# Optimization experiments

Hardware: AMD Instinct MI355X
Metric: run time of the kernel (lower is better)

## Reference

```python
import jax, jax.numpy as jnp
import numpy as np

L, D, H, N, B2 = 9, 256, 4, 1024, 4   # layers, embed dim, heads, keypoints, 2*pairs
HD = D // H
THR = 0.1
MAXM = 50


def _linear(x, W, b):
    return x @ W.T + b


def _ln(x, g, b, eps=1e-5):
    m = jnp.mean(x, -1, keepdims=True)
    v = jnp.var(x, -1, keepdims=True)
    return (x - m) * jax.lax.rsqrt(v + eps) * g + b


def _ffn(x, w1, b1, g, bb, w2, b2):
    h = _linear(x, w1, b1)
    h = jax.nn.gelu(_ln(h, g, bb), approximate=False)
    return _linear(h, w2, b2)


def _mha(q, k, v):
    b, nq, _ = q.shape
    nk = k.shape[1]
    qh = q.reshape(b, nq, H, HD)
    kh = k.reshape(b, nk, H, HD)
    vh = v.reshape(b, nk, H, HD)
    s = jnp.einsum('bqhd,bkhd->bhqk', qh, kh) * (1.0 / np.float32(np.sqrt(HD)))
    a = jax.nn.softmax(s, -1)
    return jnp.einsum('bhqk,bkhd->bqhd', a, vh).reshape(b, nq, D)


def _rotate_half(qk):  # qk: [b, n, D, 2]
    b, n, _, _ = qk.shape
    r = qk.reshape(b, n, H, HD // 2, 2, 2)
    r = jnp.stack([-r[..., 1, :], r[..., 0, :]], axis=4)
    return r.reshape(b, n, D, 2)


def _posenc(kpts, Wr):
    proj = kpts @ Wr.T                    # [b, n, HD//2]
    def expand(t):
        t = jnp.repeat(t, 2, axis=-1)     # interleave -> [b, n, HD]
        return jnp.tile(t, (1, 1, H))     # -> [b, n, D]
    return jnp.stack([expand(jnp.cos(proj)), expand(jnp.sin(proj))])  # [2, b, n, D]


def _forward(kpts, desc, posenc_Wr,
             sWqkv_w, sWqkv_b, sOut_w, sOut_b, sF1_w, sF1_b, sLN_g, sLN_b, sF2_w, sF2_b,
             cQK_w, cQK_b, cV_w, cV_b, cOut_w, cOut_b, cF1_w, cF1_b, cLN_g, cLN_b, cF2_w, cF2_b,
             fp_w, fp_b, match_w, match_b):
    enc = _posenc(kpts, posenc_Wr)
    x = desc
    idx = np.arange(B2)
    swap = idx // 2 * 2 + (1 - idx % 2)   # swap images within each pair
    for i in range(L):
        # ---- self attention with cached rotary encoding ----
        b, n, _ = x.shape
        qkv = _linear(x, sWqkv_w[i], sWqkv_b[i]).reshape(b, n, D, 3)
        qk, v = qkv[..., :2], qkv[..., 2]
        qk = enc[0][..., None] * qk + enc[1][..., None] * _rotate_half(qk)
        ctx = _mha(qk[..., 0], qk[..., 1], v)
        msg = _linear(ctx, sOut_w[i], sOut_b[i])
        x = x + _ffn(jnp.concatenate([x, msg], -1),
                     sF1_w[i], sF1_b[i], sLN_g[i], sLN_b[i], sF2_w[i], sF2_b[i])
        # ---- cross attention between images of each pair ----
        qk = _linear(x, cQK_w[i], cQK_b[i])
        v = _linear(x, cV_w[i], cV_b[i])
        m = _mha(qk, qk[swap], v[swap])
        m = _linear(m, cOut_w[i], cOut_b[i])
        x = x + _ffn(jnp.concatenate([x, m], -1),
                     cF1_w[i], cF1_b[i], cLN_g[i], cLN_b[i], cF2_w[i], cF2_b[i])
    # ---- match assignment: sigmoid log double softmax ----
    md = _linear(x, fp_w, fp_b) / (D ** 0.25)
    sim = jnp.einsum('bnd,bmd->bnm', md[0::2], md[1::2])
    z = _linear(x, match_w, match_b)      # [B2, N, 1]
    cert = jax.nn.log_sigmoid(z[0::2]) + jnp.swapaxes(jax.nn.log_sigmoid(z[1::2]), 1, 2)
    return jax.nn.log_softmax(sim, 2) + jax.nn.log_softmax(sim, 1) + cert


def _filter_matches(scores):
    B = scores.shape[0]
    m0 = jnp.argmax(scores, 2)
    m1 = jnp.argmax(scores, 1)
    mscores = jnp.exp(jnp.max(scores, 2))
    mutual = jnp.arange(N)[None, :] == jnp.take_along_axis(m1, m0, 1)
    masked = mscores * ((mscores > THR) & mutual).astype(mscores.dtype)
    topk_scores, topk_idx = jax.lax.top_k(masked, MAXM)
    topk_m1 = jnp.take_along_axis(m0, topk_idx, 1)
    b_idx = jnp.broadcast_to(jnp.arange(B)[:, None], (B, MAXM))
    matches = jnp.stack([b_idx, topk_idx, topk_m1], 2)
    return matches[0], topk_scores[0]


def setup_inputs() -> dict:
    key = jax.random.key(0)
    ks = iter(jax.random.split(key, 48))
    def w(shape, scale=0.02):
        return jax.random.normal(next(ks), shape, jnp.float32) * scale
    inp = {
        'kpts': jax.random.normal(next(ks), (B2, N, 2), jnp.float32),
        'desc': jax.random.normal(next(ks), (B2, N, D), jnp.float32),
        'posenc_Wr': w((HD // 2, 2), 1.0),  # std = gamma**-2 = 1
        'sWqkv_w': w((L, 3 * D, D)), 'sWqkv_b': w((L, 3 * D)),
        'sOut_w': w((L, D, D)), 'sOut_b': w((L, D)),
        'sF1_w': w((L, 2 * D, 2 * D)), 'sF1_b': w((L, 2 * D)),
        'sLN_g': jnp.ones((L, 2 * D), jnp.float32), 'sLN_b': jnp.zeros((L, 2 * D), jnp.float32),
        'sF2_w': w((L, D, 2 * D)), 'sF2_b': w((L, D)),
        'cQK_w': w((L, D, D)), 'cQK_b': w((L, D)),
        'cV_w': w((L, D, D)), 'cV_b': w((L, D)),
        'cOut_w': w((L, D, D)), 'cOut_b': w((L, D)),
        'cF1_w': w((L, 2 * D, 2 * D)), 'cF1_b': w((L, 2 * D)),
        'cLN_g': jnp.ones((L, 2 * D), jnp.float32), 'cLN_b': jnp.zeros((L, 2 * D), jnp.float32),
        'cF2_w': w((L, D, 2 * D)), 'cF2_b': w((L, D)),
        'fp_w': w((D, D)), 'fp_b': w((D,)),
        'match_w': w((1, D)), 'match_b': w((1,)),
    }
    return inp


def reference(kpts, desc, posenc_Wr,
              sWqkv_w, sWqkv_b, sOut_w, sOut_b, sF1_w, sF1_b, sLN_g, sLN_b, sF2_w, sF2_b,
              cQK_w, cQK_b, cV_w, cV_b, cOut_w, cOut_b, cF1_w, cF1_b, cLN_g, cLN_b, cF2_w, cF2_b,
              fp_w, fp_b, match_w, match_b):
    scores = _forward(kpts, desc, posenc_Wr,
                      sWqkv_w, sWqkv_b, sOut_w, sOut_b, sF1_w, sF1_b, sLN_g, sLN_b, sF2_w, sF2_b,
                      cQK_w, cQK_b, cV_w, cV_b, cOut_w, cOut_b, cF1_w, cF1_b, cLN_g, cLN_b, cF2_w, cF2_b,
                      fp_w, fp_b, match_w, match_b)
    matches, mscores = _filter_matches(scores)
    return scores, matches, mscores
```

## Files before the change

### kernel.cpp

```cpp
#include <hip/hip_runtime.h>
#include <hip/hip_bf16.h>
#include <math.h>

typedef __hip_bfloat16 bf16;
typedef unsigned short ushort;
typedef unsigned int u32;
typedef __attribute__((ext_vector_type(8))) short s8b;
typedef __attribute__((ext_vector_type(4))) short s4b;
typedef __attribute__((ext_vector_type(4))) float f4v;

#define Nc 1024
#define Dc 256
#define MA 4096

__device__ __forceinline__ float tofl(float v){ return v; }
__device__ __forceinline__ float tofl(bf16 v){ return __bfloat162float(v); }

__device__ __forceinline__ ushort rneu(float f){
  unsigned u = __float_as_uint(f);
  unsigned r = (u + 0x7fffu + ((u>>16)&1u)) >> 16;
  return (ushort)r;
}
__device__ __forceinline__ float ubf(ushort h){ return __uint_as_float(((unsigned)h)<<16); }

__device__ __forceinline__ float fexp2(float x){
#if __has_builtin(__builtin_amdgcn_exp2f)
  return __builtin_amdgcn_exp2f(x);
#else
  return exp2f(x);
#endif
}

__global__ void k_detect(const void* p, int* flag){
  if(threadIdx.x==0 && blockIdx.x==0){
    *flag = (((const ushort*)p)[0] == 0x3F80) ? 0 : 1;
  }
}

template<typename TIN>
__device__ void gemm_body(const float* A, const TIN* B, const TIN* bias, float* C,
                          int M, int Nout, int K, int lda, int ldb, int ldc,
                          float alpha, int accum, int dolog){
  __shared__ float As[32][33];
  __shared__ float Bs[32][33];
  int tx = threadIdx.x, ty = threadIdx.y;
  int tid = ty*16 + tx;
  int n0 = blockIdx.x*32, m0 = blockIdx.y*32;
  int lr = tid >> 3;
  int lc = (tid & 7) * 4;
  float acc00=0.f, acc01=0.f, acc10=0.f, acc11=0.f;
  for(int kk=0; kk<K; kk+=32){
    int m = m0 + lr, n = n0 + lr;
#pragma unroll
    for(int j=0;j<4;j++){
      int k = kk + lc + j;
      As[lr][lc+j] = (m < M && k < K) ? A[(size_t)m*lda + k] : 0.f;
      Bs[lr][lc+j] = (n < Nout && k < K) ? tofl(B[(size_t)n*ldb + k]) : 0.f;
    }
    __syncthreads();
#pragma unroll
    for(int k=0;k<32;k++){
      float a0 = As[ty][k],   a1 = As[ty+16][k];
      float b0 = Bs[tx][k],   b1 = Bs[tx+16][k];
      acc00 += a0*b0; acc01 += a0*b1; acc10 += a1*b0; acc11 += a1*b1;
    }
    __syncthreads();
  }
#define STORE(mm,nn,acc) do{ int m_=(mm), n_=(nn); if(m_<M && n_<Nout){ \
    float r = (acc) + (bias ? tofl(bias[n_]) : 0.f); r *= alpha; \
    if(dolog) r = fminf(r,0.f) - log1pf(expf(-fabsf(r))); \
    if(accum) C[(size_t)m_*ldc + n_] += r; else C[(size_t)m_*ldc + n_] = r; } }while(0)
  STORE(m0+ty,    n0+tx,    acc00);
  STORE(m0+ty,    n0+tx+16, acc01);
  STORE(m0+ty+16, n0+tx,    acc10);
  STORE(m0+ty+16, n0+tx+16, acc11);
#undef STORE
}

__global__ __launch_bounds__(256)
void k_gemm_w(const int* flag, const float* A, const void* Bb, long boff,
              const void* biasb, long biasoff, float* C,
              int M, int Nout, int K, int lda, int ldb, int ldc,
              float alpha, int accum, int dolog){
  if(*flag){
    const float* B = ((const float*)Bb) + boff;
    const float* bi = biasb ? ((const float*)biasb) + biasoff : nullptr;
    gemm_body<float>(A, B, bi, C, M, Nout, K, lda, ldb, ldc, alpha, accum, dolog);
  }else{
    const bf16* B = ((const bf16*)Bb) + boff;
    const bf16* bi = biasb ? ((const bf16*)biasb) + biasoff : nullptr;
    gemm_body<bf16>(A, B, bi, C, M, Nout, K, lda, ldb, ldc, alpha, accum, dolog);
  }
}

template<typename TIN>
__device__ void cast2_body(const void* in_, float* x, ushort* xh, ushort* xl, int n){
  const TIN* in = (const TIN*)in_;
  int i = blockIdx.x*256 + threadIdx.x;
  if(i >= n) return;
  float f = tofl(in[i]);
  x[i] = f;
  ushort h = rneu(f);
  xh[i] = h; xl[i] = rneu(f - ubf(h));
}
__global__ void k_cast2(const int* flag, const void* in, float* x, ushort* xh, ushort* xl, int n){
  if(*flag) cast2_body<float>(in, x, xh, xl, n); else cast2_body<bf16>(in, x, xh, xl, n);
}

template<typename TIN>
__device__ void splitw_body(const void* src_, long off, ushort* dh, ushort* dl, int n){
  const TIN* src = ((const TIN*)src_) + off;
  int i = blockIdx.x*256 + threadIdx.x;
  if(i >= n) return;
  float f = tofl(src[i]);
  ushort h = rneu(f);
  dh[i] = h; dl[i] = rneu(f - ubf(h));
}
__global__ void k_splitw(const int* flag, const void* src, long off, ushort* dh, ushort* dl, int n){
  if(*flag) splitw_body<float>(src, off, dh, dl, n); else splitw_body<bf16>(src, off, dh, dl, n);
}
template<typename TIN>
__device__ void biasf_body(const void* src_, long off, float* dst, int n){
  const TIN* src = ((const TIN*)src_) + off;
  int i = blockIdx.x*256 + threadIdx.x;
  if(i < n) dst[i] = tofl(src[i]);
}
__global__ void k_biasf(const int* flag, const void* src, long off, float* dst, int n){
  if(*flag) biasf_body<float>(src, off, dst, n); else biasf_body<bf16>(src, off, dst, n);
}

template<typename TIN>
__device__ void rotcs_body(const void* kpts_, const void* Wr_, float* cs){
  int i = blockIdx.x*256 + threadIdx.x;
  if(i >= MA*32) return;
  int m = i >> 5, p = i & 31;
  const TIN* kpts = (const TIN*)kpts_;
  const TIN* Wr   = (const TIN*)Wr_;
  float kx = tofl(kpts[m*2]), ky = tofl(kpts[m*2+1]);
  float proj = kx*tofl(Wr[p*2]) + ky*tofl(Wr[p*2+1]);
  cs[(size_t)m*64 + p*2    ] = cosf(proj);
  cs[(size_t)m*64 + p*2 + 1] = sinf(proj);
}
__global__ void k_rotcs(const int* flag, const void* kpts, const void* Wr, float* cs){
  if(*flag) rotcs_body<float>(kpts, Wr, cs); else rotcs_body<bf16>(kpts, Wr, cs);
}

template<typename TIN>
__device__ void wsl_body(int L, const void* p0,const void* p1,const void* p2,const void* p3,
                         const void* p4,const void* p5,const void* p6,const void* p7,const void* p8,
                         const void* b0,const void* b1,const void* b2,const void* b3,const void* b4,
                         const void* b5,const void* b6,const void* b7,const void* b8,
                         ushort* WH, ushort* WL, float* WB){
  int idx = blockIdx.x*256 + threadIdx.x;
  if(idx < 311296){
    int i = idx*4;
    const TIN* s;
    if(i < 196608){
      int nr = i >> 8, col = i & 255;
      int sr = (nr < 256) ? nr*3 : (nr < 512) ? (nr-256)*3+1 : (nr-512)*3+2;
      s = (const TIN*)p0 + (size_t)L*196608 + sr*256 + col;
    }
    else if(i < 262144)  s = (const TIN*)p1 + (size_t)L*65536  + (i-196608);
    else if(i < 524288)  s = (const TIN*)p2 + (size_t)L*262144 + (i-262144);
    else if(i < 655360)  s = (const TIN*)p3 + (size_t)L*131072 + (i-524288);
    else if(i < 720896)  s = (const TIN*)p4 + (size_t)L*65536  + (i-655360);
    else if(i < 786432)  s = (const TIN*)p5 + (size_t)L*65536  + (i-720896);
    else if(i < 851968)  s = (const TIN*)p6 + (size_t)L*65536  + (i-786432);
    else if(i < 1114112) s = (const TIN*)p7 + (size_t)L*262144 + (i-851968);
    else                 s = (const TIN*)p8 + (size_t)L*131072 + (i-1114112);
    float f[4];
    if constexpr(sizeof(TIN) == 4){
      f4v v = *(const f4v*)s;
      f[0]=v[0]; f[1]=v[1]; f[2]=v[2]; f[3]=v[3];
    } else {
      s4b v = *(const s4b*)s;
#pragma unroll
      for(int j=0;j<4;j++) f[j] = __uint_as_float(((u32)(ushort)v[j])<<16);
    }
    s4b hv, lv;
#pragma unroll
    for(int j=0;j<4;j++){
      ushort h = rneu(f[j]);
      hv[j] = (short)h;
      lv[j] = (short)rneu(f[j] - ubf(h));
    }
    *(s4b*)&WH[i] = hv;
    *(s4b*)&WL[i] = lv;
  } else if(idx < 311296 + 3328){
    int j = idx - 311296;
    const TIN* s;
    if(j < 768){
      int sj = (j < 256) ? j*3 : (j < 512) ? (j-256)*3+1 : (j-512)*3+2;
      s = (const TIN*)b0 + (size_t)L*768 + sj;
    }
    else if(j < 1024)  s = (const TIN*)b1 + (size_t)L*256 + (j-768);
    else if(j < 1536)  s = (const TIN*)b2 + (size_t)L*512 + (j-1024);
    else if(j < 1792)  s = (const TIN*)b3 + (size_t)L*256 + (j-1536);
    else if(j < 2048)  s = (const TIN*)b4 + (size_t)L*256 + (j-1792);
    else if(j < 2304)  s = (const TIN*)b5 + (size_t)L*256 + (j-2048);
    else if(j < 2560)  s = (const TIN*)b6 + (size_t)L*256 + (j-2304);
    else if(j < 3072)  s = (const TIN*)b7 + (size_t)L*512 + (j-2560);
    else               s = (const TIN*)b8 + (size_t)L*256 + (j-3072);
    WB[j] = tofl(*s);
  }
}
__global__ void k_wsplit(const int* flag, int L0, long strW, long strB,
    const void* p0,const void* p1,const void* p2,const void* p3,const void* p4,
    const void* p5,const void* p6,const void* p7,const void* p8,
    const void* b0,const void* b1,const void* b2,const void* b3,const void* b4,
    const void* b5,const void* b6,const void* b7,const void* b8,
    ushort* WH, ushort* WL, float* WB){
  int L = L0 + blockIdx.y;
  ushort* WHl = WH + (size_t)blockIdx.y*strW;
  ushort* WLl = WL + (size_t)blockIdx.y*strW;
  float*  WBl = WB + (size_t)blockIdx.y*strB;
  if(*flag) wsl_body<float>(L,p0,p1,p2,p3,p4,p5,p6,p7,p8,b0,b1,b2,b3,b4,b5,b6,b7,b8,WHl,WLl,WBl);
  else      wsl_body<bf16>(L,p0,p1,p2,p3,p4,p5,p6,p7,p8,b0,b1,b2,b3,b4,b5,b6,b7,b8,WHl,WLl,WBl);
}

__global__ __launch_bounds__(256)
void k_wcomb(ushort* WH, ushort* WL, float* WB, long strW, long strB){
  __shared__ __align__(16) float w1b[16][256];
  int strip = blockIdx.x;
  int c = blockIdx.y;
  int L = c >> 1, br = c & 1;
  size_t wbase = (size_t)L*strW + (br ? 851968 : 262144);
  size_t obase = (size_t)L*strW + (br ? 786432 : 196608);
  float* WBl  = WB + (size_t)L*strB;
  float* b1   = WBl + (br ? 2560 : 1024);
  float* bout = WBl + (br ? 2304 : 768);
  int t = threadIdx.x;
  int o0 = strip*16;
  for(int idx = t; idx < 16*256; idx += 256){
    int o = idx >> 8, j = idx & 255;
    size_t s = wbase + (size_t)(o0+o)*512 + 256 + j;
    w1b[o][j] = ubf(WH[s]) + ubf(WL[s]);
  }
  __syncthreads();
  float acc[16];
#pragma unroll
  for(int o=0;o<16;o++) acc[o] = 0.f;
  for(int j=0;j<256;j+=8){
    size_t s0 = obase + (size_t)j*256 + t;
    float wv[8];
#pragma unroll
    for(int r=0;r<8;r++){
      wv[r] = ubf(WH[s0 + r*256]) + ubf(WL[s0 + r*256]);
    }
#pragma unroll
    for(int o=0;o<16;o++){
      f4v wa = *(const f4v*)&w1b[o][j];
      f4v wb = *(const f4v*)&w1b[o][j+4];
      acc[o] += wa[0]*wv[0] + wa[1]*wv[1] + wa[2]*wv[2] + wa[3]*wv[3]
              + wb[0]*wv[4] + wb[1]*wv[5] + wb[2]*wv[6] + wb[3]*wv[7];
    }
  }
#pragma unroll
  for(int o=0;o<16;o++){
    size_t s = wbase + (size_t)(o0+o)*512 + 256 + t;
    ushort hh = rneu(acc[o]);
    WH[s] = hh; WL[s] = rneu(acc[o] - ubf(hh));
  }
  if(t < 16){
    float s = 0.f;
    for(int j=0;j<256;j++) s += w1b[t][j]*bout[j];
    b1[o0 + t] += s;
  }
}

template<int MT>
__global__ __launch_bounds__(256)
void k_gemm_mxT(const ushort* __restrict__ Ah, const ushort* __restrict__ Al,
                const ushort* __restrict__ A2h, const ushort* __restrict__ A2l, int lda,
                const ushort* __restrict__ Bh, const ushort* __restrict__ Bl, int ldb,
                const float* __restrict__ bias, float alpha,
                float* C, int ldc, int accum,
                ushort* Ch, ushort* Cl, int lds,
                ushort* keh, ushort* kel, const float* __restrict__ cs,
                ushort* vth, ushort* vtl,
                int K, int mode){
  constexpr int MFR = MT/16;
  constexpr int NACC = MFR*2;
  constexpr int MFH = MFR/2;
  __shared__ __align__(16) ushort LB[(2*MT+128)*72];
  int t = threadIdx.x;
  int n0 = blockIdx.x*64, m0 = blockIdx.y*MT;
  int w = t>>6, lane = t&63, quad = lane>>4, l15 = lane&15;
  int kg = w>>1, nh = w&1;
  int brow = t>>2, bc16 = (t&3)*16;
  int arow = (MT==64) ? (t>>2) : (t>>3);
  int acol = (MT==64) ? ((t&3)*16) : ((t&7)*8);
  f4v acc[NACC];
  f4v zz = {0.f,0.f,0.f,0.f};
#pragma unroll
  for(int j=0;j<NACC;j++) acc[j] = zz;
  int rounds = K >> 6;

  s8b r0,r1,r2,r3,r4,r5,r6,r7;
  auto gload = [&](int r){
    int k0 = r*64;
    const ushort* ah = Ah; const ushort* al = Al; int kloc = k0;
    if(A2h && k0 >= 256){ ah = A2h; al = A2l; kloc = k0 - 256; }
    const ushort* aph = &ah[(size_t)(m0+arow)*lda + kloc + acol];
    const ushort* apl = &al[(size_t)(m0+arow)*lda + kloc + acol];
    const ushort* bph = &Bh[(size_t)(n0+brow)*ldb + k0 + bc16];
    const ushort* bpl = &Bl[(size_t)(n0+brow)*ldb + k0 + bc16];
    r0 = *(const s8b*)aph;
    r2 = *(const s8b*)apl;
    if(MT==64){ r1 = *(const s8b*)(aph+8); r3 = *(const s8b*)(apl+8); }
    r4 = *(const s8b*)bph;   r5 = *(const s8b*)(bph+8);
    r6 = *(const s8b*)bpl;   r7 = *(const s8b*)(bpl+8);
  };
  auto writeS = [&](){
    *(s8b*)&LB[(arow)*72 + acol]        = r0;
    *(s8b*)&LB[(MT+arow)*72 + acol]     = r2;
    if(MT==64){
      *(s8b*)&LB[(arow)*72 + acol+8]    = r1;
      *(s8b*)&LB[(MT+arow)*72 + acol+8] = r3;
    }
    *(s8b*)&LB[(2*MT+brow)*72 + bc16]      = r4;
    *(s8b*)&LB[(2*MT+brow)*72 + bc16+8]    = r5;
    *(s8b*)&LB[(2*MT+64+brow)*72 + bc16]   = r6;
    *(s8b*)&LB[(2*MT+64+brow)*72 + bc16+8] = r7;
  };

  gload(0);
  for(int r=0; r<rounds; r++){
    __syncthreads();
    writeS();
    __syncthreads();
    s8b afh[MFR], afl[MFR], bfh[2], bfl[2];
#pragma unroll
    for(int mf=0;mf<MFR;mf++){
      afh[mf] = *(s8b*)&LB[(mf*16+l15)*72 + kg*32+quad*8];
      afl[mf] = *(s8b*)&LB[(MT+mf*16+l15)*72 + kg*32+quad*8];
    }
#pragma unroll
    for(int nf=0;nf<2;nf++){
      bfh[nf] = *(s8b*)&LB[(2*MT+nh*32+nf*16+l15)*72 + kg*32+quad*8];
      bfl[nf] = *(s8b*)&LB[(2*MT+64+nh*32+nf*16+l15)*72 + kg*32+quad*8];
    }
    if(r+1 < rounds) gload(r+1);
#pragma unroll
    for(int mf=0;mf<MFR;mf++){
#pragma unroll
      for(int nf=0;nf<2;nf++){
        int a = mf*2+nf;
        acc[a] = __builtin_amdgcn_mfma_f32_16x16x32_bf16(afh[mf], bfh[nf], acc[a], 0,0,0);
        acc[a] = __builtin_amdgcn_mfma_f32_16x16x32_bf16(afh[mf], bfl[nf], acc[a], 0,0,0);
        acc[a] = __builtin_amdgcn_mfma_f32_16x16x32_bf16(afl[mf], bfh[nf], acc[a], 0,0,0);
      }
    }
  }
  __syncthreads();
  f4v* scr = (f4v*)LB;
#pragma unroll
  for(int f=0;f<NACC;f++) scr[(w*NACC+f)*64 + lane] = acc[f];
  __syncthreads();
  int pw = w^2;
#pragma unroll
  for(int f=0;f<NACC;f++){
    f4v o = scr[(pw*NACC+f)*64 + lane];
    acc[f] += o;
  }

  bool vblk = (mode == 1 && n0 >= 512) || (mode == 3 && n0 >= 256);
  if(vblk){
    __syncthreads();
    u32* tp = (u32*)LB;
#pragma unroll
    for(int mi=0;mi<MFH;mi++){
      int mf = kg*MFH + mi;
#pragma unroll
      for(int nf=0;nf<2;nf++){
        f4v a = acc[mf*2+nf];
#pragma unroll
        for(int rr=0;rr<4;rr++){
          int ml = mf*16 + quad*4 + rr;
          int nl = nh*32 + nf*16 + l15;
          float val = a[rr];
          if(bias) val += bias[n0 + nl];
          val *= alpha;
          ushort hh = rneu(val);
          ushort ll = rneu(val - ubf(hh));
          tp[nl*(MT+1) + ml] = (u32)hh | ((u32)ll << 16);
        }
      }
    }
    __syncthreads();
    int b = m0 >> 10;
    int mloc = m0 & 1023;
    int d0 = n0 - ((mode == 1) ? 512 : 256);
    constexpr int NPASS = (MT==64) ? 2 : 1;
#pragma unroll
    for(int pass=0; pass<NPASS; pass++){
      int row, col;
      if(MT==64){ row = (t>>3) + pass*32; col = (t&7)*8; }
      else      { row = t>>2;             col = (t&3)*8; }
      int d = d0 + row;
      u32 c0=tp[row*(MT+1)+col+0], c1=tp[row*(MT+1)+col+1], c2=tp[row*(MT+1)+col+2], c3=tp[row*(MT+1)+col+3];
      u32 c4=tp[row*(MT+1)+col+4], c5=tp[row*(MT+1)+col+5], c6=tp[row*(MT+1)+col+6], c7=tp[row*(MT+1)+col+7];
      s8b hi, lo;
      hi[0]=(short)(c0&0xffff); lo[0]=(short)(c0>>16);
      hi[1]=(short)(c1&0xffff); lo[1]=(short)(c1>>16);
      hi[2]=(short)(c2&0xffff); lo[2]=(short)(c2>>16);
      hi[3]=(short)(c3&0xffff); lo[3]=(short)(c3>>16);
      hi[4]=(short)(c4&0xffff); lo[4]=(short)(c4>>16);
      hi[5]=(short)(c5&0xffff); lo[5]=(short)(c5>>16);
      hi[6]=(short)(c6&0xffff); lo[6]=(short)(c6>>16);
      hi[7]=(short)(c7&0xffff); lo[7]=(short)(c7>>16);
      size_t go = ((size_t)((b*4 + (d>>6))*64 + (d&63)))*1024 + mloc + col;
      *(s8b*)&vth[go] = hi;
      *(s8b*)&vtl[go] = lo;
    }
    return;
  }

#pragma unroll
  for(int mi=0;mi<MFH;mi++){
    int mf = kg*MFH + mi;
#pragma unroll
    for(int nf=0;nf<2;nf++){
      f4v a = acc[mf*2+nf];
#pragma unroll
      for(int rr=0;rr<4;rr++){
        int m = m0 + mf*16 + quad*4 + rr;
        int n = n0 + nh*32 + nf*16 + l15;
        float val = a[rr];
        if(bias) val += bias[n];
        val *= alpha;
        if(mode == 1){
          int d = (n < 256) ? n : (n - 256);
          const float* csp = cs + (size_t)m*64 + (d & 62);
          float cc = csp[0], ssn = csp[1];
          float pv = __shfl_xor(val, 1);
          float rv = (d & 1) ? (cc*val + ssn*pv) : (cc*val - ssn*pv);
          ushort hh = rneu(rv);
          ushort* dh = (n < 256) ? Ch : keh;
          ushort* dl = (n < 256) ? Cl : kel;
          size_t gi = (size_t)m*256 + d;
          dh[gi] = hh; dl[gi] = rneu(rv - ubf(hh));
        } else if(mode == 3){
          ushort hh = rneu(val);
          Ch[(size_t)m*256 + n] = hh;
          Cl[(size_t)m*256 + n] = rneu(val - ubf(hh));
        } else {
          if(C){
            size_t ci = (size_t)m*ldc + n;
            if(accum) val += C[ci];
            C[ci] = val;
          }
          if(Ch){
            ushort hh = rneu(val);
            Ch[(size_t)m*lds + n] = hh;
            Cl[(size_t)m*lds + n] = rneu(val - ubf(hh));
          }
        }
      }
    }
  }
}

#define FSC 0.18033688011112042f
__global__ __launch_bounds__(256)
void k_flashmx(const ushort* __restrict__ qh_, const ushort* __restrict__ ql_,
               const ushort* __restrict__ kh_, const ushort* __restrict__ kl_,
               const ushort* __restrict__ vth_, const ushort* __restrict__ vtl_,
               ushort* __restrict__ cth, ushort* __restrict__ ctl, int bxor,
               float* __restrict__ PO, float* __restrict__ PML, int nch){
  int qt = blockIdx.x, z = blockIdx.y, ch = blockIdx.z;
  int b = z>>2, h = z&3;
  int bk = b ^ bxor;
  __shared__ __align__(16) ushort Kh[64][72], Kl[64][72], Vh[64][72], Vl[64][72];
  int t = threadIdx.x, w = t>>6, lane = t&63, quad = lane>>4, l15 = lane&15;
  ushort* Psw = &Kh[w*16][0];
  s8b qfh[2], qfl[2];
  {
    size_t row = (size_t)b*1024 + qt*64 + w*16 + l15;
    const ushort* qrh = qh_ + row*256 + h*64;
    const ushort* qrl = ql_ + row*256 + h*64;
    qfh[0] = *(const s8b*)(qrh + quad*8);
    qfh[1] = *(const s8b*)(qrh + 32 + quad*8);
    qfl[0] = *(const s8b*)(qrl + quad*8);
    qfl[1] = *(const s8b*)(qrl + 32 + quad*8);
  }
  float m_i[4] = {-1e30f,-1e30f,-1e30f,-1e30f};
  float l_i[4] = {0.f,0.f,0.f,0.f};
  f4v O[4];
  f4v zz = {0.f,0.f,0.f,0.f};
#pragma unroll
  for(int dt=0;dt<4;dt++) O[dt] = zz;

  s8b rK0,rK1,rK2,rK3, rV0,rV1,rV2,rV3;
  auto stage_load = [&](int kt){
#pragma unroll
    for(int i=0;i<4;i++){
      int c = t + i*256;
      int half = c>>9, row = (c>>3)&63, o8 = (c&7)*8;
      const s8b* src = (const s8b*)((half ? kl_ : kh_) +
                       ((size_t)(bk*1024 + kt*64 + row))*256 + h*64 + o8);
      if(i==0) rK0=*src; else if(i==1) rK1=*src; else if(i==2) rK2=*src; else rK3=*src;
    }
#pragma unroll
    for(int i=0;i<4;i++){
      int c = t + i*256;
      int half = c>>9, d = (c>>3)&63, o8 = (c&7)*8;
      const s8b* src = (const s8b*)((half ? vtl_ : vth_) +
                       ((size_t)((bk*4+h)*64 + d))*1024 + kt*64 + o8);
      if(i==0) rV0=*src; else if(i==1) rV1=*src; else if(i==2) rV2=*src; else rV3=*src;
    }
  };
  auto stage_write = [&](){
#pragma unroll
    for(int i=0;i<4;i++){
      int c = t + i*256;
      int half = c>>9, row = (c>>3)&63, o8 = (c&7)*8;
      s8b v = (i==0)?rK0:(i==1)?rK1:(i==2)?rK2:rK3;
      if(half) *(s8b*)&Kl[row][o8] = v;
      else     *(s8b*)&Kh[row][o8] = v;
    }
#pragma unroll
    for(int i=0;i<4;i++){
      int c = t + i*256;
      int half = c>>9, d = (c>>3)&63, o8 = (c&7)*8;
      s8b v = (i==0)?rV0:(i==1)?rV1:(i==2)?rV2:rV3;
      if(half) *(s8b*)&Vl[d][o8] = v;
      else     *(s8b*)&Vh[d][o8] = v;
    }
  };

  int ktn = 16/nch;
  int kt0 = ch*ktn;
  stage_load(kt0);
  for(int kt=kt0; kt<kt0+ktn; kt++){
    __syncthreads();
    stage_write();
    __syncthreads();
    if(kt+1 < kt0+ktn) stage_load(kt+1);
    f4v s[4];
#pragma unroll
    for(int nt=0;nt<4;nt++) s[nt] = zz;
#pragma unroll
    for(int nt=0;nt<4;nt++){
#pragma unroll
      for(int k2=0;k2<2;k2++){
        s8b fbh = *(s8b*)&Kh[nt*16+l15][k2*32 + quad*8];
        s8b fbl = *(s8b*)&Kl[nt*16+l15][k2*32 + quad*8];
        s[nt] = __builtin_amdgcn_mfma_f32_16x16x32_bf16(qfh[k2], fbh, s[nt], 0,0,0);
        s[nt] = __builtin_amdgcn_mfma_f32_16x16x32_bf16(qfh[k2], fbl, s[nt], 0,0,0);
        s[nt] = __builtin_amdgcn_mfma_f32_16x16x32_bf16(qfl[k2], fbh, s[nt], 0,0,0);
      }
    }
    __syncthreads();
#pragma unroll
    for(int rr=0;rr<4;rr++){
      float v0=s[0][rr]*FSC, v1=s[1][rr]*FSC, v2=s[2][rr]*FSC, v3=s[3][rr]*FSC;
      float mx = fmaxf(fmaxf(v0,v1), fmaxf(v2,v3));
      mx = fmaxf(mx, __shfl_xor(mx,1));
      mx = fmaxf(mx, __shfl_xor(mx,2));
      mx = fmaxf(mx, __shfl_xor(mx,4));
      mx = fmaxf(mx, __shfl_xor(mx,8));
      float mnew = fmaxf(m_i[rr], mx);
      float al = fexp2(m_i[rr] - mnew);
      float p0 = fexp2(v0-mnew), p1 = fexp2(v1-mnew), p2 = fexp2(v2-mnew), p3 = fexp2(v3-mnew);
      float ls = p0+p1+p2+p3;
      ls += __shfl_xor(ls,1);
      ls += __shfl_xor(ls,2);
      ls += __shfl_xor(ls,4);
      ls += __shfl_xor(ls,8);
      l_i[rr] = l_i[rr]*al + ls;
      m_i[rr] = mnew;
#pragma unroll
      for(int dt=0;dt<4;dt++) O[dt][rr] *= al;
      int prow = quad*4 + rr;
      Psw[prow*72 +  0 + l15] = rneu(p0);
      Psw[prow*72 + 16 + l15] = rneu(p1);
      Psw[prow*72 + 32 + l15] = rneu(p2);
      Psw[prow*72 + 48 + l15] = rneu(p3);
    }
    s8b pf0 = *(s8b*)&Psw[l15*72 + quad*8];
    s8b pf1 = *(s8b*)&Psw[l15*72 + 32 + quad*8];
#pragma unroll
    for(int dt=0;dt<4;dt++){
#pragma unroll
      for(int k2=0;k2<2;k2++){
        s8b fvh = *(s8b*)&Vh[dt*16+l15][k2*32 + quad*8];
        s8b fvl = *(s8b*)&Vl[dt*16+l15][k2*32 + quad*8];
        s8b pf = k2 ? pf1 : pf0;
        O[dt] = __builtin_amdgcn_mfma_f32_16x16x32_bf16(pf, fvh, O[dt], 0,0,0);
        O[dt] = __builtin_amdgcn_mfma_f32_16x16x32_bf16(pf, fvl, O[dt], 0,0,0);
      }
    }
  }
  if(nch == 1){
#pragma unroll
    for(int rr=0;rr<4;rr++){
      float inv = 1.f / l_i[rr];
      int row = qt*64 + w*16 + quad*4 + rr;
#pragma unroll
      for(int dt=0;dt<4;dt++){
        float val = O[dt][rr]*inv;
        size_t gi = ((size_t)b*1024 + row)*256 + h*64 + dt*16 + l15;
        ushort hh = rneu(val);
        cth[gi] = hh; ctl[gi] = rneu(val - ubf(hh));
      }
    }
  } else {
    size_t tb = (size_t)(z*16+qt)*nch + ch;
    float* po  = PO  + tb*4096;
    float* pml = PML + tb*128;
#pragma unroll
    for(int rr=0;rr<4;rr++){
      int row = w*16 + quad*4 + rr;
#pragma unroll
      for(int dt=0;dt<4;dt++){
        po[row*64 + dt*16 + l15] = O[dt][rr];
      }
      if(l15 == 0){
        pml[row]      = m_i[rr];
        pml[64 + row] = l_i[rr];
      }
    }
  }
}

__global__ __launch_bounds__(256)
void k_fmerge(const float* __restrict__ PO, const float* __restrict__ PML,
              ushort* __restrict__ cth, ushort* __restrict__ ctl){
  int qt = blockIdx.x, z = blockIdx.y;
  int b = z>>2, h = z&3;
  int t = threadIdx.x;
  int row = t>>2, dg = (t&3)*16;
  size_t tb0 = (size_t)(z*16+qt)*4;
  float m0 = PML[(tb0+0)*128 + row], m1 = PML[(tb0+1)*128 + row];
  float m2 = PML[(tb0+2)*128 + row], m3 = PML[(tb0+3)*128 + row];
  float M = fmaxf(fmaxf(m0,m1), fmaxf(m2,m3));
  float w0 = fexp2(m0-M), w1 = fexp2(m1-M), w2 = fexp2(m2-M), w3 = fexp2(m3-M);
  float L = PML[(tb0+0)*128 + 64 + row]*w0 + PML[(tb0+1)*128 + 64 + row]*w1
          + PML[(tb0+2)*128 + 64 + row]*w2 + PML[(tb0+3)*128 + 64 + row]*w3;
  float inv = 1.f/L;
  const f4v* p0 = (const f4v*)(PO + (tb0+0)*4096 + row*64 + dg);
  const f4v* p1 = (const f4v*)(PO + (tb0+1)*4096 + row*64 + dg);
  const f4v* p2 = (const f4v*)(PO + (tb0+2)*4096 + row*64 + dg);
  const f4v* p3 = (const f4v*)(PO + (tb0+3)*4096 + row*64 + dg);
  size_t gi = ((size_t)b*1024 + qt*64 + row)*256 + h*64 + dg;
#pragma unroll
  for(int j=0;j<4;j++){
    f4v o = p0[j]*w0 + p1[j]*w1 + p2[j]*w2 + p3[j]*w3;
#pragma unroll
    for(int e=0;e<4;e++){
      float val = o[e]*inv;
      ushort hh = rneu(val);
      cth[gi + j*4 + e] = hh;
      ctl[gi + j*4 + e] = rneu(val - ubf(hh));
    }
  }
}

template<typename TIN>
__device__ void ln2_body(const float* h, ushort* hh, ushort* hl, const TIN* g, const TIN* bb){
  __shared__ float ws8[8];
  int r = blockIdx.x; int t = threadIdx.x;
  int w = t>>6, lane = t&63;
  const float* row = h + (size_t)r*512;
  float a = row[t], b_ = row[t+256];
  float s = a + b_;
#pragma unroll
  for(int off=1; off<64; off<<=1) s += __shfl_xor(s, off);
  if(lane==0) ws8[w] = s;
  __syncthreads();
  float mean = (ws8[0]+ws8[1]+ws8[2]+ws8[3])*(1.f/512.f);
  float da = a-mean, db = b_-mean;
  float v = da*da + db*db;
#pragma unroll
  for(int off=1; off<64; off<<=1) v += __shfl_xor(v, off);
  if(lane==0) ws8[4+w] = v;
  __syncthreads();
  float rstd = rsqrtf((ws8[4]+ws8[5]+ws8[6]+ws8[7])*(1.f/512.f) + 1e-5f);
  float na = da*rstd*tofl(g[t])     + tofl(bb[t]);
  float nb = db*rstd*tofl(g[t+256]) + tofl(bb[t+256]);
  float ga = 0.5f*na*(1.f + erff(na*0.70710678f));
  float gb = 0.5f*nb*(1.f + erff(nb*0.70710678f));
  size_t base = (size_t)r*512;
  ushort u0 = rneu(ga); hh[base+t] = u0; hl[base+t] = rneu(ga - ubf(u0));
  ushort u1 = rneu(gb); hh[base+t+256] = u1; hl[base+t+256] = rneu(gb - ubf(u1));
}
__global__ void k_ln_gelu2(const int* flag, const float* h, ushort* hh, ushort* hl,
                           const void* gb, long goff, const void* bbb, long boff){
  if(*flag) ln2_body<float>(h, hh, hl, ((const float*)gb)+goff, ((const float*)bbb)+boff);
  else      ln2_body<bf16>(h, hh, hl, ((const bf16*)gb)+goff, ((const bf16*)bbb)+boff);
}

__global__ void k_lse_cols2(const float* __restrict__ simbase, float* __restrict__ clseb){
  __shared__ float Rm[16][16], Rs[16][16];
  int blk = blockIdx.x;
  int p = blk >> 6, bx = blk & 63;
  const float* sim = simbase + (size_t)p*1048576;
  float* clse = clseb + p*1024;
  int t = threadIdx.x;
  int c = t & 15, s = t >> 4;
  int col = bx*16 + c;
  const float* base = sim + col;
  float mx = -1e30f, sum = 0.f;
  for(int n=s*64; n<s*64+64; n++){
    float v = base[(size_t)n*1024];
    if(v > mx){ sum = sum*expf(mx - v) + 1.f; mx = v; }
    else sum += expf(v - mx);
  }
  Rm[s][c] = mx; Rs[s][c] = sum; __syncthreads();
  for(int off=8; off>0; off>>=1){
    if(s < off){
      float m2 = Rm[s+off][c], s2 = Rs[s+off][c];
      float m1 = Rm[s][c], s1 = Rs[s][c];
      float m = fmaxf(m1, m2);
      Rm[s][c] = m;
      Rs[s][c] = s1*expf(m1-m) + s2*expf(m2-m);
    }
    __syncthreads();
  }
  if(s == 0) clse[col] = Rm[0][c] + logf(Rs[0][c]);
}

__global__ __launch_bounds__(256)
void k_final2r(float* __restrict__ out,
               const float* __restrict__ clse, const float* __restrict__ lsg,
               int* __restrict__ m0, float* __restrict__ msc){
  __shared__ float ws4[4];
  __shared__ float bsum[4];
  int blk = blockIdx.x;
  int p = blk >> 10, n = blk & 1023;
  int t = threadIdx.x;
  int w = t>>6, lane = t&63;
  size_t base = (size_t)blk*1024;
  float v0 = out[base+t], v1 = out[base+t+256], v2 = out[base+t+512], v3 = out[base+t+768];
  float mx = fmaxf(fmaxf(v0,v1),fmaxf(v2,v3));
#pragma unroll
  for(int off=1; off<64; off<<=1) mx = fmaxf(mx, __shfl_xor(mx, off));
  if(lane==0) ws4[w] = mx;
  __syncthreads();
  float bm = fmaxf(fmaxf(ws4[0],ws4[1]),fmaxf(ws4[2],ws4[3]));
  float s = expf(v0-bm)+expf(v1-bm)+expf(v2-bm)+expf(v3-bm);
#pragma unroll
  for(int off=1; off<64; off<<=1) s += __shfl_xor(s, off);
  if(lane==0) bsum[w] = s;
  __syncthreads();
  float rl = bm + logf(bsum[0]+bsum[1]+bsum[2]+bsum[3]);
  float lgn = lsg[p*2048 + n];
  const float* lgm = lsg + p*2048 + 1024;
  const float* cl = clse + p*1024;
  float bv = -1e30f; int bi = 0;
  float nv;
  int m;
  m = t;     nv = 2.f*v0 - rl - cl[m] + lgn + lgm[m]; out[base+m] = nv; if(nv > bv){ bv = nv; bi = m; }
  m = t+256; nv = 2.f*v1 - rl - cl[m] + lgn + lgm[m]; out[base+m] = nv; if(nv > bv){ bv = nv; bi = m; }
  m = t+512; nv = 2.f*v2 - rl - cl[m] + lgn + lgm[m]; out[base+m] = nv; if(nv > bv){ bv = nv; bi = m; }
  m = t+768; nv = 2.f*v3 - rl - cl[m] + lgn + lgm[m]; out[base+m] = nv; if(nv > bv){ bv = nv; bi = m; }
  if(p) return;
#pragma unroll
  for(int off=1; off<64; off<<=1){
    float v2_ = __shfl_xor(bv, off); int i2 = __shfl_xor(bi, off);
    if(v2_ > bv || (v2_ == bv && i2 < bi)){ bv = v2_; bi = i2; }
  }
  __shared__ float wv[4]; __shared__ int wi[4];
  if(lane==0){ wv[w]=bv; wi[w]=bi; }
  __syncthreads();
  if(t==0){
#pragma unroll
    for(int k=1;k<4;k++){
      if(wv[k] > wv[0] || (wv[k]==wv[0] && wi[k] < wi[0])){ wv[0]=wv[k]; wi[0]=wi[k]; }
    }
    m0[n] = wi[0]; msc[n] = expf(wv[0]);
  }
}

__global__ void k_amax_cols2(const float* __restrict__ sc, int* __restrict__ m1){
  __shared__ float Rv[16][16]; __shared__ int Ri[16][16];
  int t = threadIdx.x;
  int c = t & 15, s = t >> 4;
  int col = blockIdx.x*16 + c;
  float bv = -1e30f; int bi = 0;
  for(int n=s*64; n<s*64+64; n++){
    float v = sc[(size_t)n*1024 + col];
    if(v > bv){ bv = v; bi = n; }
  }
  Rv[s][c]=bv; Ri[s][c]=bi; __syncthreads();
  for(int off=8; off>0; off>>=1){
    if(s < off){
      if(Rv[s+off][c] > Rv[s][c]){ Rv[s][c]=Rv[s+off][c]; Ri[s][c]=Ri[s+off][c]; }
    }
    __syncthreads();
  }
  if(s == 0) m1[col] = Ri[0][c];
}

__global__ __launch_bounds__(128)
void k_topk(const int* __restrict__ m0, const int* __restrict__ m1,
            const float* __restrict__ msc, float* __restrict__ out){
  __shared__ float V[1024];
  int t = threadIdx.x;
  for(int i2=t; i2<1024; i2+=128){
    float mv = msc[i2];
    V[i2] = (mv > 0.1f && m1[m0[i2]] == i2) ? mv : 0.f;
  }
  __syncthreads();
  int i = blockIdx.x*128 + t;
  float vi = V[i];
  int r = 0;
#pragma unroll 8
  for(int j=0;j<1024;j++){
    float vj = V[j];
    r += (vj > vi || (vj == vi && j < i)) ? 1 : 0;
  }
  if(r < 50){
    out[2*Nc*Nc + r*3 + 0] = 0.f;
    out[2*Nc*Nc + r*3 + 1] = (float)i;
    out[2*Nc*Nc + r*3 + 2] = (float)m0[i];
    out[2*Nc*Nc + 150 + r] = vi;
  }
}

extern "C" void kernel_launch(void* const* d_in, const int* in_sizes, int n_in,
                              void* d_out, int out_size, void* d_ws, size_t ws_size,
                              hipStream_t stream){
  const void* kpts    = d_in[0];
  const void* desc    = d_in[1];
  const void* Wr      = d_in[2];
  const void* sWqkv_w = d_in[3];
  const void* sWqkv_b = d_in[4];
  const void* sOut_w  = d_in[5];
  const void* sOut_b  = d_in[6];
  const void* sF1_w   = d_in[7];
  const void* sF1_b   = d_in[8];
  const void* sLN_g   = d_in[9];
  const void* sLN_b   = d_in[10];
  const void* sF2_w   = d_in[11];
  const void* sF2_b   = d_in[12];
  const void* cQK_w   = d_in[13];
  const void* cQK_b   = d_in[14];
  const void* cV_w    = d_in[15];
  const void* cV_b    = d_in[16];
  const void* cOut_w  = d_in[17];
  const void* cOut_b  = d_in[18];
  const void* cF1_w   = d_in[19];
  const void* cF1_b   = d_in[20];
  const void* cLN_g   = d_in[21];
  const void* cLN_b   = d_in[22];
  const void* cF2_w   = d_in[23];
  const void* cF2_b   = d_in[24];
  const void* fp_w    = d_in[25];
  const void* fp_b    = d_in[26];
  const void* match_w = d_in[27];
  const void* match_b = d_in[28];

  float* ws  = (float*)d_ws;
  float* out = (float*)d_out;
  int* flag = (int*)d_ws;
  float* zbuf = ws + 64;
  float* clse = ws + 6208;
  float* msc  = ws + 12352;
  int*   m0i  = (int*)(ws + 13376);
  int*   m1i  = (int*)(ws + 14400);

  bool presplit = ws_size >= (size_t)20759552*4 + 1024;
  size_t wW = presplit ? 5603328 : 622592;
  size_t wB = presplit ? 32768   : 4096;

  size_t o = 16384;
  ushort* WH = (ushort*)(ws + o); o += wW;
  ushort* WL = (ushort*)(ws + o); o += wW;
  float*  WB = ws + o;            o += wB;
  ushort* fpWH = (ushort*)(ws + o); o += 32768;
  ushort* fpWL = (ushort*)(ws + o); o += 32768;
  float*  fpB  = ws + o;            o += 1024;
  float*  x  = ws + o;              o += 1048576;
  ushort* xh = (ushort*)(ws + o);   o += 524288;
  ushort* xl = (ushort*)(ws + o);   o += 524288;
  float*  hbuf = ws + o;            o += 2097152;
  ushort* qsh = (ushort*)(ws + o);  o += 524288;
  ushort* qsl = (ushort*)(ws + o);  o += 524288;
  ushort* ksh = (ushort*)(ws + o);  o += 524288;
  ushort* ksl = (ushort*)(ws + o);  o += 524288;
  ushort* vth = (ushort*)(ws + o);  o += 524288;
  ushort* vtl = (ushort*)(ws + o);  o += 524288;
  ushort* cth = (ushort*)(ws + o);  o += 524288;
  ushort* ctl = (ushort*)(ws + o);  o += 524288;
  ushort* mgh = (ushort*)(ws + o);  o += 524288;
  ushort* mgl = (ushort*)(ws + o);  o += 524288;
  ushort* hsh = qsh;
  ushort* hsl = ksh;
  ushort* mdh = cth;
  ushort* mdl = ctl;

  float* cs = out;

  float* PO  = ws + o;
  float* PML = ws + o + 4194304;
  int nch = (ws_size >= (size_t)(20759552 + 4194304 + 131072)*4 + 1024) ? 4 : 1;

  auto MX = [&](const ushort* Ah, const ushort* Al, const ushort* A2h, const ushort* A2l,
                int lda, const ushort* Bh, const ushort* Bl, int ldb,
                const float* bias, float alpha, float* C, int ldc, int accum,
                ushort* Ch, ushort* Cl, int lds,
                ushort* keh, ushort* kel, ushort* vh, ushort* vl,
                int M, int Nout, int K, int mode, int mt){
    dim3 g(Nout/64, M/mt);
    if(mt == 32)
      k_gemm_mxT<32><<<g, 256, 0, stream>>>(Ah,Al,A2h,A2l,lda,Bh,Bl,ldb,bias,alpha,C,ldc,accum,
                                            Ch,Cl,lds,keh,kel,cs,vh,vl,K,mode);
    else
      k_gemm_mxT<64><<<g, 256, 0, stream>>>(Ah,Al,A2h,A2l,lda,Bh,Bl,ldb,bias,alpha,C,ldc,accum,
                                            Ch,Cl,lds,keh,kel,cs,vh,vl,K,mode);
  };
  auto FLASH = [&](const ushort* qh, const ushort* ql, const ushort* kh, const ushort* kl,
                   int bxor){
    k_flashmx<<<dim3(16,16,nch), 256, 0, stream>>>(qh,ql,kh,kl,vth,vtl, cth,ctl, bxor,
                                                   PO, PML, nch);
    if(nch == 4) k_fmerge<<<dim3(16,16), 256, 0, stream>>>(PO, PML, cth, ctl);
  };

  k_detect<<<1, 64, 0, stream>>>(sLN_g, flag);
  k_splitw<<<(65536+255)/256, 256, 0, stream>>>(flag, fp_w, 0, fpWH, fpWL, 65536);
  k_biasf<<<1, 256, 0, stream>>>(flag, fp_b, 0, fpB, 256);
  k_cast2<<<(MA*Dc+255)/256, 256, 0, stream>>>(flag, desc, x, xh, xl, MA*Dc);
  k_rotcs<<<(MA*32+255)/256, 256, 0, stream>>>(flag, kpts, Wr, cs);

  if(presplit){
    dim3 g((311296+3328+255)/256, 9);
    k_wsplit<<<g, 256, 0, stream>>>(flag, 0, 1245184, 3328,
      sWqkv_w, sOut_w, sF1_w, sF2_w, cQK_w, cV_w, cOut_w, cF1_w, cF2_w,
      sWqkv_b, sOut_b, sF1_b, sF2_b, cQK_b, cV_b, cOut_b, cF1_b, cF2_b,
      WH, WL, WB);
    k_wcomb<<<dim3(32, 18), 256, 0, stream>>>(WH, WL, WB, 1245184, 3328);
  }

  for(int i=0;i<9;i++){
    if(!presplit){
      dim3 g((311296+3328+255)/256, 1);
      k_wsplit<<<g, 256, 0, stream>>>(flag, i, 0, 0,
        sWqkv_w, sOut_w, sF1_w, sF2_w, cQK_w, cV_w, cOut_w, cF1_w, cF2_w,
        sWqkv_b, sOut_b, sF1_b, sF2_b, cQK_b, cV_b, cOut_b, cF1_b, cF2_b,
        WH, WL, WB);
      k_wcomb<<<dim3(32, 2), 256, 0, stream>>>(WH, WL, WB, 0, 0);
    }
    const ushort* WHl = presplit ? WH + (size_t)i*1245184 : WH;
    const ushort* WLl = presplit ? WL + (size_t)i*1245184 : WL;
    const float*  WBl = presplit ? WB + (size_t)i*3328    : WB;

    MX(xh,xl,nullptr,nullptr,256, WHl+0,WLl+0,256, WBl+0, 1.f,
       nullptr,0,0, qsh,qsl,0, ksh,ksl, vth,vtl, MA,768,256, 1, 32);
    FLASH(qsh,qsl,ksh,ksl, 0);
    MX(xh,xl,cth,ctl,256, WHl+262144,WLl+262144,512, WBl+1024, 1.f,
       hbuf,512,0, nullptr,nullptr,0, nullptr,nullptr, nullptr,nullptr, MA,512,512, 0, 32);
    k_ln_gelu2<<<MA, 256, 0, stream>>>(flag, hbuf, hsh, hsl, sLN_g, (long)i*512, sLN_b, (long)i*512);
    MX(hsh,hsl,nullptr,nullptr,512, WHl+524288,WLl+524288,512, WBl+1536, 1.f,
       x,256,1, xh,xl,256, nullptr,nullptr, nullptr,nullptr, MA,256,512, 0, 32);
    MX(xh,xl,nullptr,nullptr,256, WHl+655360,WLl+655360,256, WBl+1792, 1.f,
       nullptr,0,0, qsh,qsl,0, nullptr,nullptr, vth,vtl, MA,512,256, 3, 32);
    FLASH(qsh,qsl,qsh,qsl, 1);
    MX(xh,xl,cth,ctl,256, WHl+851968,WLl+851968,512, WBl+2560, 1.f,
       hbuf,512,0, nullptr,nullptr,0, nullptr,nullptr, nullptr,nullptr, MA,512,512, 0, 32);
    k_ln_gelu2<<<MA, 256, 0, stream>>>(flag, hbuf, hsh, hsl, cLN_g, (long)i*512, cLN_b, (long)i*512);
    MX(hsh,hsl,nullptr,nullptr,512, WHl+1114112,WLl+1114112,512, WBl+3072, 1.f,
       x,256,1, xh,xl,256, nullptr,nullptr, nullptr,nullptr, MA,256,512, 0, 32);
  }

  MX(xh,xl,nullptr,nullptr,256, fpWH,fpWL,256, fpB, 0.25f,
     nullptr,0,0, mdh,mdl,256, nullptr,nullptr, nullptr,nullptr, MA,256,256, 0, 32);
  k_gemm_w<<<dim3(1,128), dim3(16,16), 0, stream>>>(flag, x, match_w, 0, match_b, 0,
                                                    zbuf, MA, 1, 256, 256, 256, 1, 1.f, 0, 1);
  MX(mdh,mdl,nullptr,nullptr,256, mdh + (size_t)1024*256, mdl + (size_t)1024*256, 256,
     nullptr, 1.f, out,1024,0, nullptr,nullptr,0, nullptr,nullptr, nullptr,nullptr, 1024,1024,256, 0, 32);
  MX(mdh + (size_t)2048*256, mdl + (size_t)2048*256,nullptr,nullptr,256,
     mdh + (size_t)3072*256, mdl + (size_t)3072*256, 256,
     nullptr, 1.f, out+1048576,1024,0, nullptr,nullptr,0, nullptr,nullptr, nullptr,nullptr, 1024,1024,256, 0, 32);

  k_lse_cols2<<<128, 256, 0, stream>>>(out, clse);
  k_final2r<<<2048, 256, 0, stream>>>(out, clse, zbuf, m0i, msc);
  k_amax_cols2<<<64, 256, 0, stream>>>(out, m1i);
  k_topk<<<8, 128, 0, stream>>>(m0i, m1i, msc, out);
}
```

Before: 1.861 ms.

## Fold output projection into FFN weights using MFMA GEMM instead of scalar kernel

```diff
diff --git a/kernel.cpp b/kernel.cpp
--- a/kernel.cpp
+++ b/kernel.cpp
@@ -154,22 +154,26 @@
   int idx = blockIdx.x*256 + threadIdx.x;
   if(idx < 311296){
     int i = idx*4;
-    const TIN* s;
+    const TIN* s = nullptr;
+    const TIN* tb = nullptr; int trow = 0, tcol = 0;
     if(i < 196608){
       int nr = i >> 8, col = i & 255;
       int sr = (nr < 256) ? nr*3 : (nr < 512) ? (nr-256)*3+1 : (nr-512)*3+2;
       s = (const TIN*)p0 + (size_t)L*196608 + sr*256 + col;
     }
-    else if(i < 262144)  s = (const TIN*)p1 + (size_t)L*65536  + (i-196608);
+    else if(i < 262144){ int li = i-196608; tb = (const TIN*)p1 + (size_t)L*65536; trow = li>>8; tcol = li&255; }
     else if(i < 524288)  s = (const TIN*)p2 + (size_t)L*262144 + (i-262144);
     else if(i < 655360)  s = (const TIN*)p3 + (size_t)L*131072 + (i-524288);
     else if(i < 720896)  s = (const TIN*)p4 + (size_t)L*65536  + (i-655360);
     else if(i < 786432)  s = (const TIN*)p5 + (size_t)L*65536  + (i-720896);
-    else if(i < 851968)  s = (const TIN*)p6 + (size_t)L*65536  + (i-786432);
+    else if(i < 851968){ int li = i-786432; tb = (const TIN*)p6 + (size_t)L*65536; trow = li>>8; tcol = li&255; }
     else if(i < 1114112) s = (const TIN*)p7 + (size_t)L*262144 + (i-851968);
     else                 s = (const TIN*)p8 + (size_t)L*131072 + (i-1114112);
     float f[4];
-    if constexpr(sizeof(TIN) == 4){
+    if(tb){
+#pragma unroll
+      for(int j=0;j<4;j++) f[j] = tofl(tb[(size_t)(tcol+j)*256 + trow]);
+    } else if constexpr(sizeof(TIN) == 4){
       f4v v = *(const f4v*)s;
       f[0]=v[0]; f[1]=v[1]; f[2]=v[2]; f[3]=v[3];
     } else {
@@ -219,53 +223,29 @@
 }
 
 __global__ __launch_bounds__(256)
-void k_wcomb(ushort* WH, ushort* WL, float* WB, long strW, long strB){
-  __shared__ __align__(16) float w1b[16][256];
-  int strip = blockIdx.x;
+void k_bcomb(const ushort* __restrict__ WH, const ushort* __restrict__ WL,
+             float* WB, long strW, long strB){
+  __shared__ float bo[256];
+  int bx = blockIdx.x;
   int c = blockIdx.y;
   int L = c >> 1, br = c & 1;
   size_t wbase = (size_t)L*strW + (br ? 851968 : 262144);
-  size_t obase = (size_t)L*strW + (br ? 786432 : 196608);
-  float* WBl  = WB + (size_t)L*strB;
-  float* b1   = WBl + (br ? 2560 : 1024);
-  float* bout = WBl + (br ? 2304 : 768);
+  float* WBl = WB + (size_t)L*strB;
+  float* b1 = WBl + (br ? 2560 : 1024);
+  const float* bout = WBl + (br ? 2304 : 768);
   int t = threadIdx.x;
-  int o0 = strip*16;
-  for(int idx = t; idx < 16*256; idx += 256){
-    int o = idx >> 8, j = idx & 255;
-    size_t s = wbase + (size_t)(o0+o)*512 + 256 + j;
-    w1b[o][j] = ubf(WH[s]) + ubf(WL[s]);
-  }
+  bo[t] = bout[t];
   __syncthreads();
-  float acc[16];
-#pragma unroll
-  for(int o=0;o<16;o++) acc[o] = 0.f;
-  for(int j=0;j<256;j+=8){
-    size_t s0 = obase + (size_t)j*256 + t;
-    float wv[8];
-#pragma unroll
-    for(int r=0;r<8;r++){
-      wv[r] = ubf(WH[s0 + r*256]) + ubf(WL[s0 + r*256]);
-    }
-#pragma unroll
-    for(int o=0;o<16;o++){
-      f4v wa = *(const f4v*)&w1b[o][j];
-      f4v wb = *(const f4v*)&w1b[o][j+4];
-      acc[o] += wa[0]*wv[0] + wa[1]*wv[1] + wa[2]*wv[2] + wa[3]*wv[3]
-              + wb[0]*wv[4] + wb[1]*wv[5] + wb[2]*wv[6] + wb[3]*wv[7];
-    }
-  }
-#pragma unroll
-  for(int o=0;o<16;o++){
-    size_t s = wbase + (size_t)(o0+o)*512 + 256 + t;
-    ushort hh = rneu(acc[o]);
-    WH[s] = hh; WL[s] = rneu(acc[o] - ubf(hh));
-  }
-  if(t < 16){
-    float s = 0.f;
-    for(int j=0;j<256;j++) s += w1b[t][j]*bout[j];
-    b1[o0 + t] += s;
-  }
+  int o = bx*64 + (t>>2);
+  int p = t & 3;
+  size_t rb = wbase + (size_t)o*512 + 256;
+  float s = 0.f;
+  for(int j=p*64; j<p*64+64; j++){
+    s += (ubf(WH[rb+j]) + ubf(WL[rb+j])) * bo[j];
+  }
+  s += __shfl_xor(s,1);
+  s += __shfl_xor(s,2);
+  if(p==0) b1[o] += s;
 }
 
 template<int MT>
@@ -285,6 +265,18 @@
   __shared__ __align__(16) ushort LB[(2*MT+128)*72];
   int t = threadIdx.x;
   int n0 = blockIdx.x*64, m0 = blockIdx.y*MT;
+  size_t wofs4 = 0;
+  if(mode == 4){
+    int by = blockIdx.y;
+    int combo = by >> 4;
+    m0 = (by & 15) * MT;
+    int Lc = combo >> 1, br = combo & 1;
+    size_t basec = (size_t)Lc * (size_t)lds;
+    wofs4 = basec + (br ? 851968 : 262144) + 256;
+    size_t oofs = basec + (br ? 786432 : 196608);
+    Bh = Ah + oofs; Bl = Al + oofs; ldb = 256;
+    Ah = Ah + wofs4; Al = Al + wofs4; lda = 512;
+  }
   int w = t>>6, lane = t&63, quad = lane>>4, l15 = lane&15;
   int kg = w>>1, nh = w&1;
   int brow = t>>2, bc16 = (t&3)*16;
@@ -444,6 +436,11 @@
           ushort hh = rneu(val);
           Ch[(size_t)m*256 + n] = hh;
           Cl[(size_t)m*256 + n] = rneu(val - ubf(hh));
+        } else if(mode == 4){
+          ushort hh = rneu(val);
+          size_t gi = wofs4 + (size_t)m*512 + n;
+          Ch[gi] = hh;
+          Cl[gi] = rneu(val - ubf(hh));
         } else {
           if(C){
             size_t ci = (size_t)m*ldc + n;
@@ -890,6 +887,7 @@
   ushort* hsl = ksh;
   ushort* mdh = cth;
   ushort* mdl = ctl;
+  (void)mgh; (void)mgl;
 
   float* cs = out;
 
@@ -917,6 +915,13 @@
                                                    PO, PML, nch);
     if(nch == 4) k_fmerge<<<dim3(16,16), 256, 0, stream>>>(PO, PML, cth, ctl);
   };
+  auto FOLD = [&](int ncombo, long strW){
+    k_bcomb<<<dim3(8, ncombo), 256, 0, stream>>>(WH, WL, WB, strW, presplit ? 3328 : 0);
+    k_gemm_mxT<32><<<dim3(4, ncombo*16), 256, 0, stream>>>(
+        WH, WL, nullptr, nullptr, 0, nullptr, nullptr, 0,
+        nullptr, 1.f, nullptr, 0, 0,
+        WH, WL, (int)strW, nullptr, nullptr, cs, nullptr, nullptr, 256, 4);
+  };
 
   k_detect<<<1, 64, 0, stream>>>(sLN_g, flag);
   k_splitw<<<(65536+255)/256, 256, 0, stream>>>(flag, fp_w, 0, fpWH, fpWL, 65536);
@@ -930,7 +935,7 @@
       sWqkv_w, sOut_w, sF1_w, sF2_w, cQK_w, cV_w, cOut_w, cF1_w, cF2_w,
       sWqkv_b, sOut_b, sF1_b, sF2_b, cQK_b, cV_b, cOut_b, cF1_b, cF2_b,
       WH, WL, WB);
-    k_wcomb<<<dim3(32, 18), 256, 0, stream>>>(WH, WL, WB, 1245184, 3328);
+    FOLD(18, 1245184);
   }
 
   for(int i=0;i<9;i++){
@@ -940,7 +945,7 @@
         sWqkv_w, sOut_w, sF1_w, sF2_w, cQK_w, cV_w, cOut_w, cF1_w, cF2_w,
         sWqkv_b, sOut_b, sF1_b, sF2_b, cQK_b, cV_b, cOut_b, cF1_b, cF2_b,
         WH, WL, WB);
-      k_wcomb<<<dim3(32, 2), 256, 0, stream>>>(WH, WL, WB, 0, 0);
+      FOLD(2, 0);
     }
     const ushort* WHl = presplit ? WH + (size_t)i*1245184 : WH;
     const ushort* WLl = presplit ? WL + (size_t)i*1245184 : WL;
```

New measurement: 1.831 ms (median of 2 runs). No clear change (-1.6%).
